# Kernel tuning notes

Hardware: AMD Instinct MI355X
Metric: run time of the kernel (lower is better)

The kernel has to match this reference:

```python
import jax, jax.numpy as jnp
import numpy as np

NUM_NODES = 10000
NUM_FEAT = 32
HIDDEN = 64
OUT_FEAT = 16
NUM_EDGES = 160000
SEQ_LEN = 12
BATCH = 1


def _gcn_conv(x, W, b, row, col, n):
    # PyG GCNConv: h = D^-1/2 (A+I) D^-1/2 (x @ W) + b
    # x: (n, T, F_in), row/col: (E+n,) with self-loops already appended
    h = x @ W                                              # (n, T, H)
    deg = jax.ops.segment_sum(jnp.ones_like(col, dtype=h.dtype), col, num_segments=n)
    dis = 1.0 / jnp.sqrt(jnp.maximum(deg, 1.0))            # deg >= 1 due to self-loops
    norm = dis[row] * dis[col]                             # (E+n,)
    msg = h[row] * norm[:, None, None]                     # gather + scale
    return jax.ops.segment_sum(msg, col, num_segments=n) + b


def _lstm_layer(x, wih, whh, bih, bhh):
    # x: (N, T, F); PyTorch gate order i, f, g, o
    H = whh.shape[1]
    Nn = x.shape[0]
    bias = bih + bhh

    def step(carry, xt):
        h, c = carry
        g = xt @ wih.T + h @ whh.T + bias
        i, f, gg, o = jnp.split(g, 4, axis=-1)
        c = jax.nn.sigmoid(f) * c + jax.nn.sigmoid(i) * jnp.tanh(gg)
        h = jax.nn.sigmoid(o) * jnp.tanh(c)
        return (h, c), h

    h0 = jnp.zeros((Nn, H), x.dtype)
    c0 = jnp.zeros((Nn, H), x.dtype)
    _, ys = jax.lax.scan(step, (h0, c0), jnp.transpose(x, (1, 0, 2)))
    return jnp.transpose(ys, (1, 0, 2))                    # (N, T, H)


def setup_inputs() -> dict:
    key = jax.random.key(0)
    ks = jax.random.split(key, 16)
    s_in = 1.0 / np.sqrt(NUM_FEAT)
    s_h = 1.0 / np.sqrt(HIDDEN)
    inp = {
        "x": jax.random.normal(ks[0], (BATCH, SEQ_LEN, NUM_NODES, NUM_FEAT), jnp.float32),
        "edge_index": jax.random.randint(ks[1], (2, NUM_EDGES), 0, NUM_NODES, dtype=jnp.int64),
        "gw0": jax.random.normal(ks[2], (NUM_FEAT, HIDDEN), jnp.float32) * s_in,
        "gb0": jnp.zeros((HIDDEN,), jnp.float32),
        "gw1": jax.random.normal(ks[3], (HIDDEN, HIDDEN), jnp.float32) * s_h,
        "gb1": jnp.zeros((HIDDEN,), jnp.float32),
        "wih0": jax.random.normal(ks[4], (4 * HIDDEN, HIDDEN), jnp.float32) * s_h,
        "whh0": jax.random.normal(ks[5], (4 * HIDDEN, HIDDEN), jnp.float32) * s_h,
        "bih0": jax.random.normal(ks[6], (4 * HIDDEN,), jnp.float32) * s_h,
        "bhh0": jax.random.normal(ks[7], (4 * HIDDEN,), jnp.float32) * s_h,
        "wih1": jax.random.normal(ks[8], (4 * HIDDEN, HIDDEN), jnp.float32) * s_h,
        "whh1": jax.random.normal(ks[9], (4 * HIDDEN, HIDDEN), jnp.float32) * s_h,
        "bih1": jax.random.normal(ks[10], (4 * HIDDEN,), jnp.float32) * s_h,
        "bhh1": jax.random.normal(ks[11], (4 * HIDDEN,), jnp.float32) * s_h,
        "fc_w": jax.random.normal(ks[12], (OUT_FEAT, HIDDEN), jnp.float32) * s_h,
        "fc_b": jnp.zeros((OUT_FEAT,), jnp.float32),
    }
    return inp


def reference(x, edge_index, gw0, gb0, gw1, gb1, wih0, whh0, bih0, bhh0,
              wih1, whh1, bih1, bhh1, fc_w, fc_b):
    B, T, n, F = x.shape
    BN = B * n
    # (B, T, N, F) -> (B, N, T, F) -> (B*N, T, F); the per-timestep GCN loop in
    # the original is batched over T here (same math, edge_index is time-invariant).
    xs = jnp.transpose(x, (0, 2, 1, 3)).reshape(BN, T, F)
    loops = jnp.arange(BN, dtype=edge_index.dtype)
    row = jnp.concatenate([edge_index[0], loops])
    col = jnp.concatenate([edge_index[1], loops])
    h = jax.nn.relu(_gcn_conv(xs, gw0, gb0, row, col, BN))
    h = jax.nn.relu(_gcn_conv(h, gw1, gb1, row, col, BN))
    h = _lstm_layer(h, wih0, whh0, bih0, bhh0)
    h = _lstm_layer(h, wih1, whh1, bih1, bhh1)
    out = h[:, -1, :] @ fc_w.T + fc_b                      # last timestep only
    return out.reshape(B, n, OUT_FEAT)
```

## Files before the change

### kernel.cpp

```cpp
#include <hip/hip_runtime.h>
#include <hip/hip_bf16.h>

constexpr int kNN  = 10000;
constexpr int kTT  = 12;
constexpr int kFIN = 32;
constexpr int kHH  = 64;
constexpr int kH4  = 256;
constexpr int kOUT = 16;
constexpr int kNE  = 160000;

typedef _Float16 half8 __attribute__((ext_vector_type(8)));
typedef _Float16 half4 __attribute__((ext_vector_type(4)));
typedef _Float16 half2t __attribute__((ext_vector_type(2)));
typedef float floatx4 __attribute__((ext_vector_type(4)));

__device__ __forceinline__ float sigf(float x){ return 1.f/(1.f+__expf(-x)); }
__device__ __forceinline__ float tanh_fast(float x){
  float xc = fminf(fmaxf(x,-30.f),30.f);
  float e = __expf(-2.f*xc);
  return (1.f-e)/(1.f+e);
}

__global__ void k_detect(const int* __restrict__ ei, int* __restrict__ anyf){
  int a = 0;
  for (int i = blockIdx.x*256 + threadIdx.x; i < kNE; i += gridDim.x*256)
    a |= ei[2*i+1];
  unsigned long long m = __ballot(a != 0);
  if ((threadIdx.x & 63) == 0 && m) atomicOr(anyf, 1);
}

__global__ void k_deg(const int* __restrict__ ei, const int* __restrict__ anyf,
                      int* __restrict__ cnt){
  int e = blockIdx.x*256 + threadIdx.x;
  if (e >= kNE) return;
  int c = (anyf[0]==0) ? ei[2*(kNE+e)] : ei[kNE+e];
  atomicAdd(&cnt[c], 1);
}

__global__ void k_scan(const int* __restrict__ cnt, int* __restrict__ offs,
                       float* __restrict__ dis){
  __shared__ int part[256];
  int tid = threadIdx.x;
  const int CH = (kNN + 255)/256;
  int lo = tid*CH, hi = min(lo+CH, kNN);
  int s = 0;
  for (int i = lo; i < hi; ++i) s += cnt[i];
  part[tid] = s;
  __syncthreads();
  if (tid == 0){
    int run = 0;
    for (int i = 0; i < 256; ++i){ int v = part[i]; part[i] = run; run += v; }
  }
  __syncthreads();
  int run = part[tid];
  for (int i = lo; i < hi; ++i){ offs[i] = run; run += cnt[i]; }
  if (hi == kNN) offs[kNN] = run;
  for (int i = tid; i < kNN; i += 256) dis[i] = rsqrtf((float)(cnt[i]+1));
}

__global__ void k_scatter(const int* __restrict__ ei, const int* __restrict__ anyf,
                          const int* __restrict__ offs, int* __restrict__ cur,
                          const float* __restrict__ dis,
                          int* __restrict__ esrc, float* __restrict__ ew){
  int e = blockIdx.x*256 + threadIdx.x;
  if (e >= kNE) return;
  int f = (anyf[0]==0);
  int r = f ? ei[2*e]         : ei[e];
  int c = f ? ei[2*(kNE+e)]   : ei[kNE+e];
  int p = offs[c] + atomicAdd(&cur[c], 1);
  esrc[p] = r;
  ew[p] = dis[r]*dis[c];
}

template<int K, int N, typename TI>
__global__ __launch_bounds__(256) void k_gemm(const TI* __restrict__ in,
                      const float* __restrict__ Wg,
                      _Float16* __restrict__ out){
  constexpr int COLG = N/4;
  constexpr int ROWG = 256/COLG;
  constexpr int MR   = 4;
  constexpr int MTILE= ROWG*MR;
  constexpr int AP   = K + 4;
  __shared__ float Wl[K*N];
  __shared__ float Al[MTILE*AP];
  int tid = threadIdx.x;
  int m0 = blockIdx.x*MTILE;
  if constexpr (__is_same(TI, _Float16)){
    for (int idx = tid; idx < MTILE*K/8; idx += 256){
      int r = idx/(K/8), k8 = idx - r*(K/8);
      half8 v = *(const half8*)&in[(size_t)(m0 + r)*K + k8*8];
      float* dst = &Al[r*AP + k8*8];
      #pragma unroll
      for (int j = 0; j < 8; ++j) dst[j] = (float)v[j];
    }
  } else {
    for (int idx = tid; idx < MTILE*K/4; idx += 256){
      int r = idx/(K/4), k4 = idx - r*(K/4);
      float4 v = *(const float4*)&in[(size_t)(m0 + r)*K + k4*4];
      float* dst = &Al[r*AP + k4*4];
      dst[0]=v.x; dst[1]=v.y; dst[2]=v.z; dst[3]=v.w;
    }
  }
  for (int idx = tid; idx < K*N; idx += 256) Wl[idx] = Wg[idx];
  __syncthreads();
  int cg = tid % COLG, rg = tid / COLG;
  int c0 = cg*4, r0 = rg*MR;
  float acc[MR][4];
  #pragma unroll
  for (int r=0;r<MR;++r){acc[r][0]=0.f;acc[r][1]=0.f;acc[r][2]=0.f;acc[r][3]=0.f;}
  #pragma unroll 2
  for (int k = 0; k < K; k += 4){
    float4 wv[4];
    #pragma unroll
    for (int kk = 0; kk < 4; ++kk) wv[kk] = *(const float4*)&Wl[(k+kk)*N + c0];
    #pragma unroll
    for (int r = 0; r < MR; ++r){
      float4 a4 = *(const float4*)&Al[(r0+r)*AP + k];
      acc[r][0] = fmaf(a4.x, wv[0].x, acc[r][0]);
      acc[r][1] = fmaf(a4.x, wv[0].y, acc[r][1]);
      acc[r][2] = fmaf(a4.x, wv[0].z, acc[r][2]);
      acc[r][3] = fmaf(a4.x, wv[0].w, acc[r][3]);
      acc[r][0] = fmaf(a4.y, wv[1].x, acc[r][0]);
      acc[r][1] = fmaf(a4.y, wv[1].y, acc[r][1]);
      acc[r][2] = fmaf(a4.y, wv[1].z, acc[r][2]);
      acc[r][3] = fmaf(a4.y, wv[1].w, acc[r][3]);
      acc[r][0] = fmaf(a4.z, wv[2].x, acc[r][0]);
      acc[r][1] = fmaf(a4.z, wv[2].y, acc[r][1]);
      acc[r][2] = fmaf(a4.z, wv[2].z, acc[r][2]);
      acc[r][3] = fmaf(a4.z, wv[2].w, acc[r][3]);
      acc[r][0] = fmaf(a4.w, wv[3].x, acc[r][0]);
      acc[r][1] = fmaf(a4.w, wv[3].y, acc[r][1]);
      acc[r][2] = fmaf(a4.w, wv[3].z, acc[r][2]);
      acc[r][3] = fmaf(a4.w, wv[3].w, acc[r][3]);
    }
  }
  #pragma unroll
  for (int r = 0; r < MR; ++r){
    half4 hv;
    hv[0]=(_Float16)acc[r][0]; hv[1]=(_Float16)acc[r][1];
    hv[2]=(_Float16)acc[r][2]; hv[3]=(_Float16)acc[r][3];
    *(half4*)&out[(size_t)(m0 + r0 + r)*N + c0] = hv;
  }
}

template<bool TM>
__global__ __launch_bounds__(256) void k_agg(const _Float16* __restrict__ hin,
                     _Float16* __restrict__ hout,
                     const float* __restrict__ bias, const float* __restrict__ dis,
                     const int* __restrict__ offs, const int* __restrict__ esrc,
                     const float* __restrict__ ew){
  int wid = threadIdx.x >> 6, lane = threadIdx.x & 63;
  int gw = blockIdx.x*4 + wid;
  int tp = gw / kNN, n = gw - tp*kNN;
  int sel = lane >> 5, fp = lane & 31;
  int t = 2*tp + sel;
  const _Float16* hb = hin + (size_t)t*kNN*kHH;
  float d = dis[n], ws = d*d;
  half2t sv = *(const half2t*)&hb[(size_t)n*kHH + 2*fp];
  float a0 = ws*(float)sv[0], a1 = ws*(float)sv[1];
  int e0 = offs[n], e1 = offs[n+1];
  int e = e0;
  for (; e + 8 <= e1; e += 8){
    int s[8]; float w[8];
    #pragma unroll
    for (int u = 0; u < 8; ++u){ s[u] = esrc[e+u]; w[u] = ew[e+u]; }
    half2t v[8];
    #pragma unroll
    for (int u = 0; u < 8; ++u) v[u] = *(const half2t*)&hb[(size_t)s[u]*kHH + 2*fp];
    #pragma unroll
    for (int u = 0; u < 8; ++u){
      a0 = fmaf(w[u], (float)v[u][0], a0);
      a1 = fmaf(w[u], (float)v[u][1], a1);
    }
  }
  for (; e < e1; ++e){
    int su = esrc[e]; float wu = ew[e];
    half2t vu = *(const half2t*)&hb[(size_t)su*kHH + 2*fp];
    a0 = fmaf(wu, (float)vu[0], a0);
    a1 = fmaf(wu, (float)vu[1], a1);
  }
  a0 = fmaxf(a0 + bias[2*fp],   0.f);
  a1 = fmaxf(a1 + bias[2*fp+1], 0.f);
  half2t o; o[0] = (_Float16)a0; o[1] = (_Float16)a1;
  size_t oi = TM ? ((size_t)t*kNN + n)*kHH + 2*fp
                 : ((size_t)n*kTT + t)*kHH + 2*fp;
  *(half2t*)&hout[oi] = o;
}

template<bool LAST>
__global__ __launch_bounds__(256) void k_rec(const _Float16* __restrict__ xin,
                     const float* __restrict__ wih, const float* __restrict__ whh,
                     const float* __restrict__ bih, const float* __restrict__ bhh,
                     void* __restrict__ hout){
  constexpr int LP = 72;
  __shared__ _Float16 hlds[2][16*LP];
  int tid = threadIdx.x, w = tid >> 6, lane = tid & 63;
  int lo = lane & 15, hi4 = lane >> 4;
  int nb = blockIdx.x*16;

  half8 BI[4][2], BH[4][2];
  #pragma unroll
  for (int q = 0; q < 4; ++q){
    int row = q*kHH + w*16 + lo;
    #pragma unroll
    for (int kt = 0; kt < 2; ++kt){
      const float* pi = wih + (size_t)row*kHH + kt*32 + hi4*8;
      const float* ph = whh + (size_t)row*kHH + kt*32 + hi4*8;
      half8 fi, fh;
      #pragma unroll
      for (int j = 0; j < 8; ++j){ fi[j] = (_Float16)pi[j]; fh[j] = (_Float16)ph[j]; }
      BI[q][kt] = fi; BH[q][kt] = fh;
    }
  }
  float bias[4];
  #pragma unroll
  for (int q = 0; q < 4; ++q){
    int col = q*kHH + w*16 + lo;
    bias[q] = bih[col] + bhh[col];
  }

  float c[4] = {0.f,0.f,0.f,0.f};
  float hval[4];
  half8 ah[2], axn[2];

  const _Float16* xrow = xin + (size_t)(nb + lo)*kTT*kHH;
  #pragma unroll
  for (int kt = 0; kt < 2; ++kt) axn[kt] = *(const half8*)&xrow[kt*32 + hi4*8];

  for (int t = 0; t < kTT; ++t){
    half8 ax[2] = {axn[0], axn[1]};
    if (t < kTT-1){
      #pragma unroll
      for (int kt = 0; kt < 2; ++kt)
        axn[kt] = *(const half8*)&xrow[(size_t)(t+1)*kHH + kt*32 + hi4*8];
    }
    floatx4 acc[4];
    #pragma unroll
    for (int q = 0; q < 4; ++q){
      floatx4 a = {0.f,0.f,0.f,0.f};
      a = __builtin_amdgcn_mfma_f32_16x16x32_f16(ax[0], BI[q][0], a, 0,0,0);
      a = __builtin_amdgcn_mfma_f32_16x16x32_f16(ax[1], BI[q][1], a, 0,0,0);
      acc[q] = a;
    }
    if (t > 0){
      #pragma unroll
      for (int q = 0; q < 4; ++q){
        floatx4 a = acc[q];
        a = __builtin_amdgcn_mfma_f32_16x16x32_f16(ah[0], BH[q][0], a, 0,0,0);
        a = __builtin_amdgcn_mfma_f32_16x16x32_f16(ah[1], BH[q][1], a, 0,0,0);
        acc[q] = a;
      }
    }
    #pragma unroll
    for (int r = 0; r < 4; ++r){
      float gi = acc[0][r] + bias[0];
      float gf = acc[1][r] + bias[1];
      float gg = acc[2][r] + bias[2];
      float go = acc[3][r] + bias[3];
      float ii = sigf(gi), ff = sigf(gf), gt = tanh_fast(gg), oo = sigf(go);
      c[r] = ff*c[r] + ii*gt;
      hval[r] = oo * tanh_fast(c[r]);
    }
    if (t < kTT-1){
      _Float16* hb = &hlds[t & 1][0];
      #pragma unroll
      for (int r = 0; r < 4; ++r)
        hb[(hi4*4 + r)*LP + w*16 + lo] = (_Float16)hval[r];
      __syncthreads();
      const _Float16* rb = &hlds[t & 1][0];
      #pragma unroll
      for (int kt = 0; kt < 2; ++kt)
        ah[kt] = *(const half8*)&rb[lo*LP + kt*32 + hi4*8];
    }
    if (!LAST){
      _Float16* ho = (_Float16*)hout;
      #pragma unroll
      for (int r = 0; r < 4; ++r)
        ho[((size_t)(nb + hi4*4 + r)*kTT + t)*kHH + w*16 + lo] = (_Float16)hval[r];
    } else if (t == kTT-1){
      float* ho = (float*)hout;
      #pragma unroll
      for (int r = 0; r < 4; ++r)
        ho[(size_t)(nb + hi4*4 + r)*kHH + w*16 + lo] = hval[r];
    }
  }
}

__global__ void k_fc(const float* __restrict__ h, const float* __restrict__ w,
                     const float* __restrict__ b, float* __restrict__ out){
  int tid = blockIdx.x*256 + threadIdx.x;
  if (tid >= kNN*kOUT) return;
  int n = tid / kOUT, o = tid - n*kOUT;
  const float* hp = h + (size_t)n*kHH;
  const float* wp = w + o*kHH;
  float acc = b[o];
  #pragma unroll 8
  for (int j = 0; j < kHH; ++j) acc = fmaf(hp[j], wp[j], acc);
  out[tid] = acc;
}

extern "C" void kernel_launch(void* const* d_in, const int* in_sizes, int n_in,
                              void* d_out, int out_size, void* d_ws, size_t ws_size,
                              hipStream_t stream){
  const float* x    = (const float*)d_in[0];
  const int*   ei   = (const int*)  d_in[1];
  const float* gw0  = (const float*)d_in[2];
  const float* gb0  = (const float*)d_in[3];
  const float* gw1  = (const float*)d_in[4];
  const float* gb1  = (const float*)d_in[5];
  const float* wih0 = (const float*)d_in[6];
  const float* whh0 = (const float*)d_in[7];
  const float* bih0 = (const float*)d_in[8];
  const float* bhh0 = (const float*)d_in[9];
  const float* wih1 = (const float*)d_in[10];
  const float* whh1 = (const float*)d_in[11];
  const float* bih1 = (const float*)d_in[12];
  const float* bhh1 = (const float*)d_in[13];
  const float* fcw  = (const float*)d_in[14];
  const float* fcb  = (const float*)d_in[15];
  float* out = (float*)d_out;

  char* ws = (char*)d_ws;
  size_t p = 0;
  auto carve = [&](size_t bytes)->char*{
    char* r = ws + p;
    p += (bytes + 255) & ~(size_t)255;
    return r;
  };
  int*   anyf = (int*)  carve(256);
  int*   cnt  = (int*)  carve(sizeof(int)*kNN);
  int*   cur  = (int*)  carve(sizeof(int)*kNN);
  int*   offs = (int*)  carve(sizeof(int)*(kNN+1));
  float* dis  = (float*)carve(sizeof(float)*kNN);
  int*   esrc = (int*)  carve(sizeof(int)*kNE);
  float* ew   = (float*)carve(sizeof(float)*kNE);
  _Float16* bufA = (_Float16*)carve(sizeof(_Float16)*(size_t)kNN*kTT*kHH);
  _Float16* bufB = (_Float16*)carve(sizeof(_Float16)*(size_t)kNN*kTT*kHH);
  (void)ws_size; (void)in_sizes; (void)n_in; (void)out_size;

  hipMemsetAsync(anyf, 0, 256, stream);
  hipMemsetAsync(cnt, 0, sizeof(int)*kNN, stream);
  hipMemsetAsync(cur, 0, sizeof(int)*kNN, stream);
  k_detect <<<80, 256, 0, stream>>>(ei, anyf);
  k_deg    <<<(kNE+255)/256, 256, 0, stream>>>(ei, anyf, cnt);
  k_scan   <<<1, 256, 0, stream>>>(cnt, offs, dis);
  k_scatter<<<(kNE+255)/256, 256, 0, stream>>>(ei, anyf, offs, cur, dis, esrc, ew);

  k_gemm<kFIN, kHH, float><<<(kNN*kTT)/64, 256, 0, stream>>>(x, gw0, bufA);
  k_agg<true> <<<(kNN*kTT/2)/4, 256, 0, stream>>>(bufA, bufB, gb0, dis, offs, esrc, ew);
  k_gemm<kHH, kHH, _Float16><<<(kNN*kTT)/64, 256, 0, stream>>>(bufB, gw1, bufA);
  k_agg<false><<<(kNN*kTT/2)/4, 256, 0, stream>>>(bufA, bufB, gb1, dis, offs, esrc, ew);

  k_rec<false><<<kNN/16, 256, 0, stream>>>(bufB, wih0, whh0, bih0, bhh0, bufA);
  k_rec<true ><<<kNN/16, 256, 0, stream>>>(bufA, wih1, whh1, bih1, bhh1, bufB);

  k_fc<<<(kNN*kOUT+255)/256, 256, 0, stream>>>((const float*)bufB, fcw, fcb, out);
}
```

Measured before the change: 358.5 us.

## Fuse both LSTM layers and final FC into one wavefront-pipelined kernel

Merges the two LSTM recurrence kernels and the FC projection into one 512-thread kernel. Waves 0-3 run layer 0 and waves 4-7 run layer 1 one timestep behind, passing h0 through shared memory instead of writing the full layer-0 sequence to global memory. The FC runs on MFMA using the last h1 held in LDS. Three memsets become one. This removes a 15 MB intermediate round trip and two launches. The cost is a block barrier on every step shared by both layers and higher per-block register and thread usage.

Measured after the change: 343.4 us. 4.2% less time.

```diff
diff --git a/kernel.cpp b/kernel.cpp
--- a/kernel.cpp
+++ b/kernel.cpp
@@ -187,21 +187,30 @@
   *(half2t*)&hout[oi] = o;
 }
 
-template<bool LAST>
-__global__ __launch_bounds__(256) void k_rec(const _Float16* __restrict__ xin,
-                     const float* __restrict__ wih, const float* __restrict__ whh,
-                     const float* __restrict__ bih, const float* __restrict__ bhh,
-                     void* __restrict__ hout){
+__global__ __launch_bounds__(512) void k_rec2(const _Float16* __restrict__ xin,
+                     const float* __restrict__ wih0, const float* __restrict__ whh0,
+                     const float* __restrict__ bih0, const float* __restrict__ bhh0,
+                     const float* __restrict__ wih1, const float* __restrict__ whh1,
+                     const float* __restrict__ bih1, const float* __restrict__ bhh1,
+                     const float* __restrict__ fcw, const float* __restrict__ fcb,
+                     float* __restrict__ out){
   constexpr int LP = 72;
-  __shared__ _Float16 hlds[2][16*LP];
+  __shared__ _Float16 h0b[2][16*LP];
+  __shared__ _Float16 h1b[2][16*LP];
   int tid = threadIdx.x, w = tid >> 6, lane = tid & 63;
   int lo = lane & 15, hi4 = lane >> 4;
+  int layer = w >> 2, wl = w & 3;
   int nb = blockIdx.x*16;
+
+  const float* wih = layer ? wih1 : wih0;
+  const float* whh = layer ? whh1 : whh0;
+  const float* bi_ = layer ? bih1 : bih0;
+  const float* bh_ = layer ? bhh1 : bhh0;
 
   half8 BI[4][2], BH[4][2];
   #pragma unroll
   for (int q = 0; q < 4; ++q){
-    int row = q*kHH + w*16 + lo;
+    int row = q*kHH + wl*16 + lo;
     #pragma unroll
     for (int kt = 0; kt < 2; ++kt){
       const float* pi = wih + (size_t)row*kHH + kt*32 + hi4*8;
@@ -215,88 +224,107 @@
   float bias[4];
   #pragma unroll
   for (int q = 0; q < 4; ++q){
-    int col = q*kHH + w*16 + lo;
-    bias[q] = bih[col] + bhh[col];
+    int col = q*kHH + wl*16 + lo;
+    bias[q] = bi_[col] + bh_[col];
+  }
+  half8 FW[2];
+  if (w == 4){
+    #pragma unroll
+    for (int kt = 0; kt < 2; ++kt){
+      const float* pf = fcw + (size_t)lo*kHH + kt*32 + hi4*8;
+      half8 f;
+      #pragma unroll
+      for (int j = 0; j < 8; ++j) f[j] = (_Float16)pf[j];
+      FW[kt] = f;
+    }
   }
 
   float c[4] = {0.f,0.f,0.f,0.f};
-  float hval[4];
-  half8 ah[2], axn[2];
+  half8 ax[2], ah[2], axn[2];
 
   const _Float16* xrow = xin + (size_t)(nb + lo)*kTT*kHH;
-  #pragma unroll
-  for (int kt = 0; kt < 2; ++kt) axn[kt] = *(const half8*)&xrow[kt*32 + hi4*8];
-
-  for (int t = 0; t < kTT; ++t){
-    half8 ax[2] = {axn[0], axn[1]};
-    if (t < kTT-1){
-      #pragma unroll
-      for (int kt = 0; kt < 2; ++kt)
-        axn[kt] = *(const half8*)&xrow[(size_t)(t+1)*kHH + kt*32 + hi4*8];
-    }
-    floatx4 acc[4];
-    #pragma unroll
-    for (int q = 0; q < 4; ++q){
-      floatx4 a = {0.f,0.f,0.f,0.f};
-      a = __builtin_amdgcn_mfma_f32_16x16x32_f16(ax[0], BI[q][0], a, 0,0,0);
-      a = __builtin_amdgcn_mfma_f32_16x16x32_f16(ax[1], BI[q][1], a, 0,0,0);
-      acc[q] = a;
-    }
-    if (t > 0){
+  if (layer == 0){
+    #pragma unroll
+    for (int kt = 0; kt < 2; ++kt) axn[kt] = *(const half8*)&xrow[kt*32 + hi4*8];
+  }
+
+  for (int i = 0; i < 13; ++i){
+    int t = layer ? i-1 : i;
+    bool act = layer ? (i >= 1) : (i < 12);
+    if (act){
+      if (layer == 0){
+        ax[0] = axn[0]; ax[1] = axn[1];
+        if (t < kTT-1){
+          #pragma unroll
+          for (int kt = 0; kt < 2; ++kt)
+            axn[kt] = *(const half8*)&xrow[(size_t)(t+1)*kHH + kt*32 + hi4*8];
+        }
+      }
+      floatx4 acc[4];
       #pragma unroll
       for (int q = 0; q < 4; ++q){
-        floatx4 a = acc[q];
-        a = __builtin_amdgcn_mfma_f32_16x16x32_f16(ah[0], BH[q][0], a, 0,0,0);
-        a = __builtin_amdgcn_mfma_f32_16x16x32_f16(ah[1], BH[q][1], a, 0,0,0);
+        floatx4 a = {0.f,0.f,0.f,0.f};
+        a = __builtin_amdgcn_mfma_f32_16x16x32_f16(ax[0], BI[q][0], a, 0,0,0);
+        a = __builtin_amdgcn_mfma_f32_16x16x32_f16(ax[1], BI[q][1], a, 0,0,0);
         acc[q] = a;
       }
-    }
-    #pragma unroll
-    for (int r = 0; r < 4; ++r){
-      float gi = acc[0][r] + bias[0];
-      float gf = acc[1][r] + bias[1];
-      float gg = acc[2][r] + bias[2];
-      float go = acc[3][r] + bias[3];
-      float ii = sigf(gi), ff = sigf(gf), gt = tanh_fast(gg), oo = sigf(go);
-      c[r] = ff*c[r] + ii*gt;
-      hval[r] = oo * tanh_fast(c[r]);
-    }
-    if (t < kTT-1){
-      _Float16* hb = &hlds[t & 1][0];
-      #pragma unroll
-      for (int r = 0; r < 4; ++r)
-        hb[(hi4*4 + r)*LP + w*16 + lo] = (_Float16)hval[r];
-      __syncthreads();
-      const _Float16* rb = &hlds[t & 1][0];
-      #pragma unroll
-      for (int kt = 0; kt < 2; ++kt)
-        ah[kt] = *(const half8*)&rb[lo*LP + kt*32 + hi4*8];
-    }
-    if (!LAST){
-      _Float16* ho = (_Float16*)hout;
-      #pragma unroll
-      for (int r = 0; r < 4; ++r)
-        ho[((size_t)(nb + hi4*4 + r)*kTT + t)*kHH + w*16 + lo] = (_Float16)hval[r];
-    } else if (t == kTT-1){
-      float* ho = (float*)hout;
-      #pragma unroll
-      for (int r = 0; r < 4; ++r)
-        ho[(size_t)(nb + hi4*4 + r)*kHH + w*16 + lo] = hval[r];
-    }
-  }
-}
-
-__global__ void k_fc(const float* __restrict__ h, const float* __restrict__ w,
-                     const float* __restrict__ b, float* __restrict__ out){
-  int tid = blockIdx.x*256 + threadIdx.x;
-  if (tid >= kNN*kOUT) return;
-  int n = tid / kOUT, o = tid - n*kOUT;
-  const float* hp = h + (size_t)n*kHH;
-  const float* wp = w + o*kHH;
-  float acc = b[o];
-  #pragma unroll 8
-  for (int j = 0; j < kHH; ++j) acc = fmaf(hp[j], wp[j], acc);
-  out[tid] = acc;
+      if (t > 0){
+        #pragma unroll
+        for (int q = 0; q < 4; ++q){
+          floatx4 a = acc[q];
+          a = __builtin_amdgcn_mfma_f32_16x16x32_f16(ah[0], BH[q][0], a, 0,0,0);
+          a = __builtin_amdgcn_mfma_f32_16x16x32_f16(ah[1], BH[q][1], a, 0,0,0);
+          acc[q] = a;
+        }
+      }
+      _Float16* hb = layer ? &h1b[t & 1][0] : &h0b[t & 1][0];
+      #pragma unroll
+      for (int r = 0; r < 4; ++r){
+        float gi = acc[0][r] + bias[0];
+        float gf = acc[1][r] + bias[1];
+        float gg = acc[2][r] + bias[2];
+        float go = acc[3][r] + bias[3];
+        float ii = sigf(gi), ff = sigf(gf), gt = tanh_fast(gg), oo = sigf(go);
+        c[r] = ff*c[r] + ii*gt;
+        float hn = oo * tanh_fast(c[r]);
+        hb[(hi4*4 + r)*LP + wl*16 + lo] = (_Float16)hn;
+      }
+    }
+    __syncthreads();
+    if (layer == 0){
+      if (i < 11){
+        const _Float16* rb = &h0b[i & 1][0];
+        #pragma unroll
+        for (int kt = 0; kt < 2; ++kt)
+          ah[kt] = *(const half8*)&rb[lo*LP + kt*32 + hi4*8];
+      }
+    } else {
+      if (i < 12){
+        const _Float16* rb = &h0b[i & 1][0];
+        #pragma unroll
+        for (int kt = 0; kt < 2; ++kt)
+          ax[kt] = *(const half8*)&rb[lo*LP + kt*32 + hi4*8];
+      }
+      if (i >= 1 && i < 12){
+        const _Float16* rb = &h1b[(i-1) & 1][0];
+        #pragma unroll
+        for (int kt = 0; kt < 2; ++kt)
+          ah[kt] = *(const half8*)&rb[lo*LP + kt*32 + hi4*8];
+      }
+    }
+  }
+  if (w == 4){
+    const _Float16* rb = &h1b[1][0];
+    half8 a0 = *(const half8*)&rb[lo*LP + 0*32 + hi4*8];
+    half8 a1 = *(const half8*)&rb[lo*LP + 1*32 + hi4*8];
+    floatx4 a = {0.f,0.f,0.f,0.f};
+    a = __builtin_amdgcn_mfma_f32_16x16x32_f16(a0, FW[0], a, 0,0,0);
+    a = __builtin_amdgcn_mfma_f32_16x16x32_f16(a1, FW[1], a, 0,0,0);
+    float bo = fcb[lo];
+    #pragma unroll
+    for (int r = 0; r < 4; ++r)
+      out[(size_t)(nb + hi4*4 + r)*kOUT + lo] = a[r] + bo;
+  }
 }
 
 extern "C" void kernel_launch(void* const* d_in, const int* in_sizes, int n_in,
@@ -330,6 +358,7 @@
   int*   anyf = (int*)  carve(256);
   int*   cnt  = (int*)  carve(sizeof(int)*kNN);
   int*   cur  = (int*)  carve(sizeof(int)*kNN);
+  size_t zbytes = p;
   int*   offs = (int*)  carve(sizeof(int)*(kNN+1));
   float* dis  = (float*)carve(sizeof(float)*kNN);
   int*   esrc = (int*)  carve(sizeof(int)*kNE);
@@ -338,9 +367,7 @@
   _Float16* bufB = (_Float16*)carve(sizeof(_Float16)*(size_t)kNN*kTT*kHH);
   (void)ws_size; (void)in_sizes; (void)n_in; (void)out_size;
 
-  hipMemsetAsync(anyf, 0, 256, stream);
-  hipMemsetAsync(cnt, 0, sizeof(int)*kNN, stream);
-  hipMemsetAsync(cur, 0, sizeof(int)*kNN, stream);
+  hipMemsetAsync(ws, 0, zbytes, stream);
   k_detect <<<80, 256, 0, stream>>>(ei, anyf);
   k_deg    <<<(kNE+255)/256, 256, 0, stream>>>(ei, anyf, cnt);
   k_scan   <<<1, 256, 0, stream>>>(cnt, offs, dis);
@@ -351,8 +378,6 @@
   k_gemm<kHH, kHH, _Float16><<<(kNN*kTT)/64, 256, 0, stream>>>(bufB, gw1, bufA);
   k_agg<false><<<(kNN*kTT/2)/4, 256, 0, stream>>>(bufA, bufB, gb1, dis, offs, esrc, ew);
 
-  k_rec<false><<<kNN/16, 256, 0, stream>>>(bufB, wih0, whh0, bih0, bhh0, bufA);
-  k_rec<true ><<<kNN/16, 256, 0, stream>>>(bufA, wih1, whh1, bih1, bhh1, bufB);
-
-  k_fc<<<(kNN*kOUT+255)/256, 256, 0, stream>>>((const float*)bufB, fcw, fcb, out);
-}
+  k_rec2<<<kNN/16, 512, 0, stream>>>(bufB, wih0, whh0, bih0, bhh0,
+                                     wih1, whh1, bih1, bhh1, fcw, fcb, out);
+}
```
